# Optimization experiments

Measured on AMD Instinct MI355X. Metric: run time of the kernel, lower is better.

Reference implementation:

```python
import jax, jax.numpy as jnp
import numpy as np

N = 512      # hidden_size
L = 16384    # sequence length


def _make_hippo_legs(n_dim):
    # make_HiPPO_legs from the source
    b = jnp.sqrt(1.0 + 2.0 * jnp.arange(n_dim, dtype=jnp.float32))
    a = b[:, None] * b[None, :]
    a = jnp.tril(a) - jnp.diag(jnp.arange(n_dim, dtype=jnp.float32))
    return -a, b


def setup_inputs() -> dict:
    key = jax.random.key(0)
    c_key, x_key = jax.random.split(key, 2)
    A, Bv = _make_hippo_legs(N)
    B = Bv[:, None]                                   # (N, 1)
    C = jax.random.normal(c_key, (1, N), dtype=jnp.float32)
    in_x = jax.random.normal(x_key, (L,), dtype=jnp.float32)
    hidden_state = jnp.zeros((N,), dtype=jnp.float32)
    return {"in_x": in_x, "hidden_state": hidden_state, "A": A, "B": B, "C": C}


def reference(in_x, hidden_state, A, B, C):
    # discretize (bilinear / Tustin) with step = 1/L
    step = 1.0 / in_x.shape[0]
    I = jnp.eye(A.shape[0], dtype=A.dtype)
    BL = jnp.linalg.inv(I - (step / 2.0) * A)
    Ab = BL @ (I + (step / 2.0) * A)                  # (N, N)
    Bb = (BL * step) @ B                              # (N, 1)

    def step_through_time(h, x):
        # x: (1,) ; h: (N,)
        h_new = Ab @ h + Bb @ x                       # (N,)
        return h_new, C @ h_new                      # output (1,)

    new_hidden_state, output = jax.lax.scan(step_through_time, hidden_state, in_x[:, None])
    return output.squeeze(), new_hidden_state
```

## Files before the change

kernel.cpp:

```cpp
#include <hip/hip_runtime.h>

#define NDIM 512
#define LSEQ 16384
#define TCH  1024
#define PCH  16

#define DTF  (1.0f/16384.0f)
#define DT2F (0.5f/16384.0f)

__device__ __forceinline__ void gkt(float* smem,
    const float* A, int lda, const float* B, int ldb,
    float* D, int ldd, int row0, int col0, int K, float alpha)
{
    const int tid  = threadIdx.x;
    const int w    = tid >> 6;
    const int lane = tid & 63;
    const int ty = lane >> 3, tx = lane & 7;

    float* As = smem + w * 1152;
    float* Bs = As + 576;

    const int Kc    = K >> 2;
    const int steps = Kc >> 4;
    const int kbase = w * Kc;

    const int ar  = lane >> 2, acg = (lane & 3) * 4;
    const int bkr = lane >> 3, bcg = (lane & 7) * 4;
    const float* Ap0 = A + (size_t)(row0 + ar) * lda + kbase + acg;
    const float* Ap1 = Ap0 + (size_t)16 * lda;
    const float* Bp0 = B + (size_t)(kbase + bkr) * ldb + col0 + bcg;
    const float* Bp1 = Bp0 + (size_t)8 * ldb;

    float4 av0 = *(const float4*)Ap0;
    float4 av1 = *(const float4*)Ap1;
    float4 bv0 = *(const float4*)Bp0;
    float4 bv1 = *(const float4*)Bp1;

    float acc[4][4] = {};

    for (int s = 0; s < steps; ++s) {
        As[(acg + 0) * 36 + ar] = av0.x;
        As[(acg + 1) * 36 + ar] = av0.y;
        As[(acg + 2) * 36 + ar] = av0.z;
        As[(acg + 3) * 36 + ar] = av0.w;
        As[(acg + 0) * 36 + ar + 16] = av1.x;
        As[(acg + 1) * 36 + ar + 16] = av1.y;
        As[(acg + 2) * 36 + ar + 16] = av1.z;
        As[(acg + 3) * 36 + ar + 16] = av1.w;
        *(float4*)(Bs + bkr * 36 + bcg)       = bv0;
        *(float4*)(Bs + (bkr + 8) * 36 + bcg) = bv1;

        if (s + 1 < steps) {
            int ko = (s + 1) * 16;
            av0 = *(const float4*)(Ap0 + ko);
            av1 = *(const float4*)(Ap1 + ko);
            bv0 = *(const float4*)(Bp0 + (size_t)ko * ldb);
            bv1 = *(const float4*)(Bp1 + (size_t)ko * ldb);
        }

#pragma unroll
        for (int kk = 0; kk < 16; ++kk) {
            float4 a = *(const float4*)(As + kk * 36 + 4 * ty);
            float4 b = *(const float4*)(Bs + kk * 36 + 4 * tx);
            acc[0][0] += a.x * b.x; acc[0][1] += a.x * b.y; acc[0][2] += a.x * b.z; acc[0][3] += a.x * b.w;
            acc[1][0] += a.y * b.x; acc[1][1] += a.y * b.y; acc[1][2] += a.y * b.z; acc[1][3] += a.y * b.w;
            acc[2][0] += a.z * b.x; acc[2][1] += a.z * b.y; acc[2][2] += a.z * b.z; acc[2][3] += a.z * b.w;
            acc[3][0] += a.w * b.x; acc[3][1] += a.w * b.y; acc[3][2] += a.w * b.z; acc[3][3] += a.w * b.w;
        }
    }

    float* red = smem + w * 1152;
#pragma unroll
    for (int i = 0; i < 4; ++i)
        *(float4*)(red + (4 * ty + i) * 32 + 4 * tx) =
            make_float4(acc[i][0], acc[i][1], acc[i][2], acc[i][3]);
    __syncthreads();

    float4 s0 = *(const float4*)(smem + 0 * 1152 + tid * 4);
    float4 s1 = *(const float4*)(smem + 1 * 1152 + tid * 4);
    float4 s2 = *(const float4*)(smem + 2 * 1152 + tid * 4);
    float4 s3 = *(const float4*)(smem + 3 * 1152 + tid * 4);
    float4 r4 = make_float4(alpha * (s0.x + s1.x + s2.x + s3.x),
                            alpha * (s0.y + s1.y + s2.y + s3.y),
                            alpha * (s0.z + s1.z + s2.z + s3.z),
                            alpha * (s0.w + s1.w + s2.w + s3.w));
    int r = tid >> 3, c = (tid & 7) * 4;
    float* dp = D + (size_t)(row0 + r) * ldd + col0 + c;
    dp[0] = r4.x; dp[1] = r4.y; dp[2] = r4.z; dp[3] = r4.w;
}

__device__ __forceinline__ void tri_decode(int t, int& it, int& jt)
{
    it = (int)((sqrtf(8.f * (float)t + 1.f) - 1.f) * 0.5f);
    while ((it + 1) * (it + 2) / 2 <= t) ++it;
    while (it * (it + 1) / 2 > t) --it;
    jt = t - it * (it + 1) / 2;
}

__device__ __forceinline__ void scan_task(int task, const float* G,
    const float* Zold, float* Znew, const float* hs, float* Hmat,
    float* hfin, int o, int last)
{
    int wid = task * 4 + (threadIdx.x >> 6);
    int lane = threadIdx.x & 63;
    int p = wid & (PCH - 1), i = wid >> 4;
    float dot = 0.f;
    if (p >= o) {
        const float* gr = G + (size_t)i * NDIM;
        const float* zc = Zold + (size_t)(p - o) * NDIM;
        int rmax = i >> 6;
        for (int r = 0; r <= rmax; ++r) {
            int k = (r << 6) + lane;
            if (k <= i) dot += gr[k] * zc[k];
        }
#pragma unroll
        for (int off = 32; off; off >>= 1) dot += __shfl_xor(dot, off, 64);
    }
    if (lane == 0) {
        float z = Zold[(size_t)p * NDIM + i] + dot;
        Znew[(size_t)p * NDIM + i] = z;
        if (last) {
            if (p < PCH - 1) Hmat[(size_t)(p + 1) * NDIM + i] = z;
            else hfin[i] = z;
            if (p == 0) Hmat[i] = hs[i];
        }
    }
}

__global__ __launch_bounds__(256) void zero_diag(const float* __restrict__ A,
    float* __restrict__ W, float* __restrict__ P0)
{
    __shared__ float sh[64][65];
    const int t = blockIdx.x, tid = threadIdx.x;
    if (t < 8) {
        const int base = t * 64;
        for (int idx = tid; idx < 4096; idx += 256) {
            int r = idx >> 6, c = idx & 63;
            sh[r][c] = ((r == c) ? 1.f : 0.f)
                     - DT2F * A[(size_t)(base + r) * NDIM + base + c];
        }
        __syncthreads();
        if (tid < 64) {
            const int lane = tid;
            float xcol[64];
#pragma unroll
            for (int i = 0; i < 64; ++i) {
                float dot = 0.f;
#pragma unroll
                for (int k = 0; k < i; ++k) dot += sh[i][k] * xcol[k];
                xcol[i] = (((lane == i) ? 1.f : 0.f) - dot) / sh[i][i];
            }
#pragma unroll
            for (int k = 0; k < 64; ++k)
                W[(size_t)(base + k) * NDIM + base + lane] = xcol[k];
        }
    } else {
        const int q = (t - 8) >> 3, d = (t - 8) & 7;
        float* buf = P0 + (size_t)q * NDIM * NDIM;
        for (int idx = tid; idx < 4096; idx += 256) {
            int r = idx >> 6, c = idx & 63;
            if (c > r) buf[(size_t)(d * 64 + r) * NDIM + d * 64 + c] = 0.f;
        }
    }
}

__global__ __launch_bounds__(256) void pairA2(const float* __restrict__ A,
    const float* __restrict__ W, float* __restrict__ T, int s)
{
    __shared__ float smem[4608];
    int ntx = s >> 5;
    int tile = blockIdx.x;
    int it = tile / ntx, jt = tile - it * ntx;
    int o = blockIdx.y * 2 * s;
    int col0 = jt * 32, k0 = col0 & ~63;
    gkt(smem, A + (size_t)(o + s) * NDIM + o + k0, NDIM,
        W + (size_t)(o + k0) * NDIM + o, NDIM,
        T + (size_t)(o + s) * NDIM + o, NDIM,
        it * 32, col0, s - k0, 1.f);
}

__global__ __launch_bounds__(256) void pairB2(float* __restrict__ W,
    const float* __restrict__ T, int s)
{
    __shared__ float smem[4608];
    int ntx = s >> 5;
    int tile = blockIdx.x;
    int it = tile / ntx, jt = tile - it * ntx;
    int o = blockIdx.y * 2 * s;
    int ke = (it * 32 + 95) & ~63; if (ke > s) ke = s;
    gkt(smem, W + (size_t)(o + s) * NDIM + (o + s), NDIM,
        T + (size_t)(o + s) * NDIM + o, NDIM,
        W + (size_t)(o + s) * NDIM + o, NDIM,
        it * 32, jt * 32, ke, DT2F);
}

__global__ __launch_bounds__(256) void form_prep(const float* __restrict__ W,
    const float* __restrict__ Bv, const float* __restrict__ C,
    float* __restrict__ Ab, float* __restrict__ V, float* __restrict__ Crows,
    float* __restrict__ Bbc)
{
    const int b = blockIdx.x, tid = threadIdx.x;
    if (b < 256) {
        int idx = b * 256 + tid;
        int i = idx >> 7, j0 = (idx & 127) << 2;
        float4 wq = *(const float4*)(W + (size_t)i * NDIM + j0);
        float4 r = make_float4(2.f * wq.x, 2.f * wq.y, 2.f * wq.z, 2.f * wq.w);
        if (i == j0)          r.x -= 1.f;
        else if (i == j0 + 1) r.y -= 1.f;
        else if (i == j0 + 2) r.z -= 1.f;
        else if (i == j0 + 3) r.w -= 1.f;
        *(float4*)(Ab + (size_t)i * NDIM + j0) = r;
    } else if (b < 384) {
        const int wv = tid >> 6, lane = tid & 63;
        int i = (b - 256) * 4 + wv;
        float s = 0.f;
        int rmax = i >> 6;
        for (int c = 0; c <= rmax; ++c) {
            int k = (c << 6) + lane;
            if (k <= i) s += W[(size_t)i * NDIM + k] * Bv[k];
        }
#pragma unroll
        for (int off = 32; off; off >>= 1) s += __shfl_xor(s, off, 64);
        if (lane == 0) {
            float bb = DTF * s;
            V[(size_t)i * TCH] = bb;
            Bbc[i] = bb;
        }
    } else {
        Crows[tid]       = C[tid];
        Crows[tid + 256] = C[tid + 256];
    }
}

__global__ __launch_bounds__(256) void round_kernel(
    const float* __restrict__ g, float* __restrict__ gnew,
    float* __restrict__ V, float* __restrict__ Crows,
    int m, int lognx, int nz, int tailmode,
    const float* __restrict__ Gscan, const float* __restrict__ Ab,
    const float* __restrict__ x, const float* __restrict__ hs,
    const float* __restrict__ Bbc, float* __restrict__ kv,
    float* __restrict__ U, const float* __restrict__ Zin,
    float* __restrict__ Zout, float* __restrict__ Hmat,
    float* __restrict__ hfin, int o)
{
    __shared__ float smem[4608];
    const int t = blockIdx.x;
    const int tid = threadIdx.x;
    const int wv = tid >> 6, lane = tid & 63;

    if (t < 136) {
        int it, jt;
        tri_decode(t, it, jt);
        int k0 = (jt * 32) & ~63;
        int ke = (it * 32 + 95) & ~63; if (ke > NDIM) ke = NDIM;
        gkt(smem, g + k0, NDIM, g + (size_t)k0 * NDIM, NDIM,
            gnew, NDIM, it * 32, jt * 32, ke - k0, 1.f);
        return;
    }
    int u = t - 136;
    if (tailmode == 0) {
        int nmx = (m >= 32) ? (m >> 5) : 1;
        if (u < nz) {
            int it = u >> lognx, jt = u & (nmx - 1);
            int ke = (it * 32 + 95) & ~63; if (ke > NDIM) ke = NDIM;
            gkt(smem, g, NDIM, V, TCH, V + m, TCH, it * 32, jt * 32, ke, 1.f);
        } else {
            u -= nz;
            int it = u >> 4, jt = u & 15;
            int col0 = jt * 32, k0 = col0 & ~63;
            gkt(smem, Crows + k0, NDIM, g + (size_t)k0 * NDIM, NDIM,
                Crows + (size_t)m * NDIM, NDIM, it * 32, col0, NDIM - k0, 1.f);
        }
    } else if (tailmode == 1) {
        if (u < 2) {
            float* cs = smem;
            for (int k = tid; k < NDIM; k += 256)
                cs[k] = Crows[(size_t)1023 * NDIM + k];
            __syncthreads();
            int j = u * 256 + tid;
            int k0 = j & ~63;
            float acc = 0.f;
            for (int k = k0; k < NDIM; k += 4) {
                acc += cs[k]     * Ab[(size_t)k * NDIM + j]
                     + cs[k + 1] * Ab[(size_t)(k + 1) * NDIM + j]
                     + cs[k + 2] * Ab[(size_t)(k + 2) * NDIM + j]
                     + cs[k + 3] * Ab[(size_t)(k + 3) * NDIM + j];
            }
            Crows[(size_t)1024 * NDIM + j] = acc;
        } else if (u < 258) {
            int j = (u - 2) * 4 + wv;
            const float* cr = Crows + (size_t)j * NDIM;
            float dot = 0.f;
#pragma unroll
            for (int rr = 0; rr < 2; ++rr) {
                int oo = rr * 256 + lane * 4;
                float4 c4 = *(const float4*)(cr + oo);
                float4 b4 = *(const float4*)(Bbc + oo);
                dot += c4.x * b4.x + c4.y * b4.y + c4.z * b4.z + c4.w * b4.w;
            }
#pragma unroll
            for (int off = 32; off; off >>= 1) dot += __shfl_xor(dot, off, 64);
            if (lane == 0) kv[j] = dot;
        } else {
            int wid = (u - 258) * 4 + wv;
            int p = wid & (PCH - 1), i = wid >> 4;
            const float* vr = V + (size_t)i * TCH;
            const float* xc = x + p * TCH;
            float s = 0.f;
#pragma unroll
            for (int rr = 0; rr < 16; ++rr) {
                int t2 = (rr << 6) + lane;
                s += vr[TCH - 1 - t2] * xc[t2];
            }
            if (p == 0) {
                const float* gr = Gscan + (size_t)i * NDIM;
                int rmax = i >> 6;
                for (int rr = 0; rr <= rmax; ++rr) {
                    int k = (rr << 6) + lane;
                    if (k <= i) s += gr[k] * hs[k];
                }
            }
#pragma unroll
            for (int off = 32; off; off >>= 1) s += __shfl_xor(s, off, 64);
            if (lane == 0) U[(size_t)p * NDIM + i] = s;
        }
    } else {
        scan_task(u, Gscan, Zin, Zout, hs, Hmat, hfin, o, 0);
    }
}

__global__ __launch_bounds__(256) void scan_round(const float* __restrict__ G,
    const float* __restrict__ Zold, float* __restrict__ Znew,
    const float* __restrict__ hs, float* __restrict__ Hmat,
    float* __restrict__ hfin, int o, int last)
{
    scan_task(blockIdx.x, G, Zold, Znew, hs, Hmat, hfin, o, last);
}

__global__ __launch_bounds__(256) void emit(const float* __restrict__ Crows,
    const float* __restrict__ Hmat, const float* __restrict__ kv,
    const float* __restrict__ x, float* __restrict__ out)
{
    int wid = blockIdx.x * 4 + (threadIdx.x >> 6);
    int lane = threadIdx.x & 63;
    int p = wid & (PCH - 1), s = wid >> 4;
    const float* cr = Crows + (size_t)(s + 1) * NDIM;
    const float* hp = Hmat + (size_t)p * NDIM;
    float dot = 0.f;
#pragma unroll
    for (int r = 0; r < 2; ++r) {
        int o = r * 256 + lane * 4;
        float4 c = *(const float4*)(cr + o);
        float4 h = *(const float4*)(hp + o);
        dot += c.x * h.x + c.y * h.y + c.z * h.z + c.w * h.w;
    }
    const float* xc = x + p * TCH;
    int rmax = s >> 6;
    for (int r = 0; r <= rmax; ++r) {
        int t = (r << 6) + lane;
        if (t <= s) dot += kv[s - t] * xc[t];
    }
#pragma unroll
    for (int off = 32; off; off >>= 1) dot += __shfl_xor(dot, off, 64);
    if (lane == 0) out[p * TCH + s] = dot;
}

extern "C" void kernel_launch(void* const* d_in, const int* in_sizes, int n_in,
                              void* d_out, int out_size, void* d_ws, size_t ws_size,
                              hipStream_t stream)
{
    (void)in_sizes; (void)n_in; (void)out_size; (void)ws_size;
    const float* x  = (const float*)d_in[0];
    const float* hs = (const float*)d_in[1];
    const float* A  = (const float*)d_in[2];
    const float* Bv = (const float*)d_in[3];
    const float* C  = (const float*)d_in[4];
    float* out = (float*)d_out;

    const int MM = NDIM * NDIM;
    float* ws     = (float*)d_ws;
    float* Ab     = ws;
    float* P0     = Ab + MM;
    float* P1     = P0 + MM;
    float* GA     = P1 + MM;
    float* GB     = GA + MM;
    float* GC     = GB + MM;
    float* GD     = GC + MM;
    float* V      = GD + MM;
    float* Crows  = V + NDIM * TCH;
    float* CrowsW = Crows + TCH * NDIM;
    float* kv     = CrowsW + TCH * NDIM;
    float* Bbc    = kv + TCH;
    float* U      = Bbc + NDIM;
    float* Z0     = U + PCH * NDIM;
    float* Z1     = Z0 + PCH * NDIM;
    float* Hmat   = Z1 + PCH * NDIM;

    float* W = CrowsW;
    float* T = P0;

    zero_diag<<<56, 256, 0, stream>>>(A, W, P0);

    for (int s = 64; s <= 256; s <<= 1) {
        int np = NDIM / (2 * s);
        int tiles = (s >> 5) * (s >> 5);
        dim3 grid(tiles, np);
        pairA2<<<grid, 256, 0, stream>>>(A, W, T, s);
        pairB2<<<grid, 256, 0, stream>>>(W, T, s);
    }
    form_prep<<<385, 256, 0, stream>>>(W, Bv, C, Ab, V, Crows, Bbc);

    const float* g = Ab;
    float* gouts[13] = {P0, P1, P0, P1, P0, P1, P0, P1, P0, GA, GB, GC, GD};
    int m = 1;
    for (int r = 0; r < 13; ++r) {
        int nmx = (m >= 32) ? (m >> 5) : 1;
        int lognx = (r >= 5) ? (r - 5) : 0;
        int nz = (m < TCH) ? 16 * nmx : 0;
        int tailmode = 0, ntail = 0, oo = 0;
        const float* Gs = GA; const float* Zi = U; float* Zo = Z0;
        if (r == 10)      { tailmode = 1; ntail = 2306; }
        else if (r == 11) { tailmode = 2; ntail = 2048; oo = 1; }
        else if (r == 12) { tailmode = 2; ntail = 2048; oo = 2; Gs = GB;
                            Zi = Z0; Zo = Z1; }
        round_kernel<<<136 + 2 * nz + ntail, 256, 0, stream>>>(
            g, gouts[r], V, Crows, m, lognx, nz, tailmode, Gs, Ab,
            x, hs, Bbc, kv, U, Zi, Zo, Hmat, out + LSEQ, oo);
        g = gouts[r];
        m <<= 1;
    }

    scan_round<<<2048, 256, 0, stream>>>(GC, Z1, Z0, hs, Hmat, out + LSEQ, 4, 0);
    scan_round<<<2048, 256, 0, stream>>>(GD, Z0, Z1, hs, Hmat, out + LSEQ, 8, 1);

    emit<<<4096, 256, 0, stream>>>(Crows, Hmat, kv, x, out);
}
```

Baseline: 268.4 us.

## Deepen gkt register prefetch to two stages and schedule heavy tiles first

The shared GEMM-tile helper now keeps two k-steps of global loads in flight, in alternating even and odd register sets, instead of one. This hides more global-memory latency behind the FMA loop, at the cost of extra registers that may reduce occupancy. The tile-index decoding in pairA2, pairB2 and round_kernel is also reordered so that tiles with longer K ranges are dispatched first. That is meant to cut tail imbalance across blocks in the triangular workloads.

```diff
diff --git a/kernel.cpp b/kernel.cpp
--- a/kernel.cpp
+++ b/kernel.cpp
@@ -31,43 +31,65 @@
     const float* Bp0 = B + (size_t)(kbase + bkr) * ldb + col0 + bcg;
     const float* Bp1 = Bp0 + (size_t)8 * ldb;
 
-    float4 av0 = *(const float4*)Ap0;
-    float4 av1 = *(const float4*)Ap1;
-    float4 bv0 = *(const float4*)Bp0;
-    float4 bv1 = *(const float4*)Bp1;
-
     float acc[4][4] = {};
 
-    for (int s = 0; s < steps; ++s) {
-        As[(acg + 0) * 36 + ar] = av0.x;
-        As[(acg + 1) * 36 + ar] = av0.y;
-        As[(acg + 2) * 36 + ar] = av0.z;
-        As[(acg + 3) * 36 + ar] = av0.w;
-        As[(acg + 0) * 36 + ar + 16] = av1.x;
-        As[(acg + 1) * 36 + ar + 16] = av1.y;
-        As[(acg + 2) * 36 + ar + 16] = av1.z;
-        As[(acg + 3) * 36 + ar + 16] = av1.w;
-        *(float4*)(Bs + bkr * 36 + bcg)       = bv0;
-        *(float4*)(Bs + (bkr + 8) * 36 + bcg) = bv1;
-
-        if (s + 1 < steps) {
-            int ko = (s + 1) * 16;
-            av0 = *(const float4*)(Ap0 + ko);
-            av1 = *(const float4*)(Ap1 + ko);
-            bv0 = *(const float4*)(Bp0 + (size_t)ko * ldb);
-            bv1 = *(const float4*)(Bp1 + (size_t)ko * ldb);
-        }
-
-#pragma unroll
-        for (int kk = 0; kk < 16; ++kk) {
-            float4 a = *(const float4*)(As + kk * 36 + 4 * ty);
-            float4 b = *(const float4*)(Bs + kk * 36 + 4 * tx);
-            acc[0][0] += a.x * b.x; acc[0][1] += a.x * b.y; acc[0][2] += a.x * b.z; acc[0][3] += a.x * b.w;
-            acc[1][0] += a.y * b.x; acc[1][1] += a.y * b.y; acc[1][2] += a.y * b.z; acc[1][3] += a.y * b.w;
-            acc[2][0] += a.z * b.x; acc[2][1] += a.z * b.y; acc[2][2] += a.z * b.z; acc[2][3] += a.z * b.w;
-            acc[3][0] += a.w * b.x; acc[3][1] += a.w * b.y; acc[3][2] += a.w * b.z; acc[3][3] += a.w * b.w;
-        }
-    }
+    float4 aE0 = *(const float4*)Ap0;
+    float4 aE1 = *(const float4*)Ap1;
+    float4 bE0 = *(const float4*)Bp0;
+    float4 bE1 = *(const float4*)Bp1;
+    float4 aO0, aO1, bO0, bO1;
+    if (steps > 1) {
+        aO0 = *(const float4*)(Ap0 + 16);
+        aO1 = *(const float4*)(Ap1 + 16);
+        bO0 = *(const float4*)(Bp0 + (size_t)16 * ldb);
+        bO1 = *(const float4*)(Bp1 + (size_t)16 * ldb);
+    }
+
+#define GKT_STAGE(a0v,a1v,b0v,b1v)                                            \
+    As[(acg + 0) * 36 + ar] = a0v.x;  As[(acg + 1) * 36 + ar] = a0v.y;        \
+    As[(acg + 2) * 36 + ar] = a0v.z;  As[(acg + 3) * 36 + ar] = a0v.w;        \
+    As[(acg + 0) * 36 + ar + 16] = a1v.x; As[(acg + 1) * 36 + ar + 16] = a1v.y;\
+    As[(acg + 2) * 36 + ar + 16] = a1v.z; As[(acg + 3) * 36 + ar + 16] = a1v.w;\
+    *(float4*)(Bs + bkr * 36 + bcg)       = b0v;                              \
+    *(float4*)(Bs + (bkr + 8) * 36 + bcg) = b1v;
+
+#define GKT_COMPUTE                                                           \
+    _Pragma("unroll")                                                         \
+    for (int kk = 0; kk < 16; ++kk) {                                         \
+        float4 a = *(const float4*)(As + kk * 36 + 4 * ty);                   \
+        float4 b = *(const float4*)(Bs + kk * 36 + 4 * tx);                   \
+        acc[0][0] += a.x * b.x; acc[0][1] += a.x * b.y; acc[0][2] += a.x * b.z; acc[0][3] += a.x * b.w; \
+        acc[1][0] += a.y * b.x; acc[1][1] += a.y * b.y; acc[1][2] += a.y * b.z; acc[1][3] += a.y * b.w; \
+        acc[2][0] += a.z * b.x; acc[2][1] += a.z * b.y; acc[2][2] += a.z * b.z; acc[2][3] += a.z * b.w; \
+        acc[3][0] += a.w * b.x; acc[3][1] += a.w * b.y; acc[3][2] += a.w * b.z; acc[3][3] += a.w * b.w; \
+    }
+
+    int s = 0;
+    while (true) {
+        GKT_STAGE(aE0, aE1, bE0, bE1);
+        if (s + 2 < steps) {
+            int ko = (s + 2) * 16;
+            aE0 = *(const float4*)(Ap0 + ko);
+            aE1 = *(const float4*)(Ap1 + ko);
+            bE0 = *(const float4*)(Bp0 + (size_t)ko * ldb);
+            bE1 = *(const float4*)(Bp1 + (size_t)ko * ldb);
+        }
+        GKT_COMPUTE;
+        if (s + 1 >= steps) break;
+        GKT_STAGE(aO0, aO1, bO0, bO1);
+        if (s + 3 < steps) {
+            int ko = (s + 3) * 16;
+            aO0 = *(const float4*)(Ap0 + ko);
+            aO1 = *(const float4*)(Ap1 + ko);
+            bO0 = *(const float4*)(Bp0 + (size_t)ko * ldb);
+            bO1 = *(const float4*)(Bp1 + (size_t)ko * ldb);
+        }
+        GKT_COMPUTE;
+        s += 2;
+        if (s >= steps) break;
+    }
+#undef GKT_STAGE
+#undef GKT_COMPUTE
 
     float* red = smem + w * 1152;
 #pragma unroll
@@ -170,7 +192,7 @@
     __shared__ float smem[4608];
     int ntx = s >> 5;
     int tile = blockIdx.x;
-    int it = tile / ntx, jt = tile - it * ntx;
+    int jt = tile / ntx, it = tile - jt * ntx;
     int o = blockIdx.y * 2 * s;
     int col0 = jt * 32, k0 = col0 & ~63;
     gkt(smem, A + (size_t)(o + s) * NDIM + o + k0, NDIM,
@@ -185,7 +207,8 @@
     __shared__ float smem[4608];
     int ntx = s >> 5;
     int tile = blockIdx.x;
-    int it = tile / ntx, jt = tile - it * ntx;
+    int it = ntx - 1 - tile / ntx;
+    int jt = tile - (tile / ntx) * ntx;
     int o = blockIdx.y * 2 * s;
     int ke = (it * 32 + 95) & ~63; if (ke > s) ke = s;
     gkt(smem, W + (size_t)(o + s) * NDIM + (o + s), NDIM,
@@ -249,8 +272,9 @@
     const int wv = tid >> 6, lane = tid & 63;
 
     if (t < 136) {
-        int it, jt;
-        tri_decode(t, it, jt);
+        int e, j;
+        tri_decode(t, e, j);
+        int jt = j, it = 15 - e + j;
         int k0 = (jt * 32) & ~63;
         int ke = (it * 32 + 95) & ~63; if (ke > NDIM) ke = NDIM;
         gkt(smem, g + k0, NDIM, g + (size_t)k0 * NDIM, NDIM,
@@ -261,12 +285,14 @@
     if (tailmode == 0) {
         int nmx = (m >= 32) ? (m >> 5) : 1;
         if (u < nz) {
-            int it = u >> lognx, jt = u & (nmx - 1);
+            int up = nz - 1 - u;
+            int it = up >> lognx, jt = up & (nmx - 1);
             int ke = (it * 32 + 95) & ~63; if (ke > NDIM) ke = NDIM;
             gkt(smem, g, NDIM, V, TCH, V + m, TCH, it * 32, jt * 32, ke, 1.f);
         } else {
             u -= nz;
-            int it = u >> 4, jt = u & 15;
+            int nty = nmx;
+            int jt = u / nty, it = u - jt * nty;
             int col0 = jt * 32, k0 = col0 & ~63;
             gkt(smem, Crows + k0, NDIM, g + (size_t)k0 * NDIM, NDIM,
                 Crows + (size_t)m * NDIM, NDIM, it * 32, col0, NDIM - k0, 1.f);
```

Result: slower. 276.3 us (+3.0%).

## Fuse Ab/Bb formation into inverse tile epilogues and merge s=64 pair pass

Applied to the files above, without the earlier changes.

The separate form_prep pass is removed. Ab = 2W - I and Bb = dt*W*B are now written directly from the diagonal-block solve and from the off-diagonal block GEMM epilogues, with Bb accumulated via atomicAdd. The s=64 pairA2/pairB2 launches are merged into a single 4-block pair64 kernel, and the Crows copy moves into zero_diag. This cuts launches and a full pass over W. In exchange it relies on atomics and assumes Bbc/V start at zero and that the strictly upper blocks of Ab are zero-filled elsewhere.

```diff
diff --git a/kernel.cpp b/kernel.cpp
--- a/kernel.cpp
+++ b/kernel.cpp
@@ -4,13 +4,16 @@
 #define LSEQ 16384
 #define TCH  1024
 #define PCH  16
+#define MM   (NDIM * NDIM)
 
 #define DTF  (1.0f/16384.0f)
 #define DT2F (0.5f/16384.0f)
 
 __device__ __forceinline__ void gkt(float* smem,
     const float* A, int lda, const float* B, int ldb,
-    float* D, int ldd, int row0, int col0, int K, float alpha)
+    float* D, int ldd, int row0, int col0, int K, float alpha,
+    float* Abe = nullptr, float* Bbce = nullptr, float* Ve = nullptr,
+    const float* Bve = nullptr, int gr0 = -1, int gc0 = 0)
 {
     const int tid  = threadIdx.x;
     const int w    = tid >> 6;
@@ -87,6 +90,22 @@
     int r = tid >> 3, c = (tid & 7) * 4;
     float* dp = D + (size_t)(row0 + r) * ldd + col0 + c;
     dp[0] = r4.x; dp[1] = r4.y; dp[2] = r4.z; dp[3] = r4.w;
+
+    if (gr0 >= 0) {
+        int grow = gr0 + row0 + r, gcol = gc0 + col0 + c;
+        *(float4*)(Abe + (size_t)grow * NDIM + gcol) =
+            make_float4(2.f * r4.x, 2.f * r4.y, 2.f * r4.z, 2.f * r4.w);
+        float pv = r4.x * Bve[gcol]     + r4.y * Bve[gcol + 1]
+                 + r4.z * Bve[gcol + 2] + r4.w * Bve[gcol + 3];
+        pv += __shfl_xor(pv, 1, 64);
+        pv += __shfl_xor(pv, 2, 64);
+        pv += __shfl_xor(pv, 4, 64);
+        if ((tid & 7) == 0) {
+            float bb = DTF * pv;
+            atomicAdd(&Bbce[grow], bb);
+            atomicAdd(&Ve[(size_t)grow * TCH], bb);
+        }
+    }
 }
 
 __device__ __forceinline__ void tri_decode(int t, int& it, int& jt)
@@ -128,7 +147,9 @@
 }
 
 __global__ __launch_bounds__(256) void zero_diag(const float* __restrict__ A,
-    float* __restrict__ W, float* __restrict__ P0)
+    float* __restrict__ W, float* __restrict__ P0, float* __restrict__ Ab,
+    float* __restrict__ Bbc, float* __restrict__ V, float* __restrict__ Crows,
+    const float* __restrict__ Bv, const float* __restrict__ C)
 {
     __shared__ float sh[64][65];
     const int t = blockIdx.x, tid = threadIdx.x;
@@ -150,17 +171,59 @@
                 for (int k = 0; k < i; ++k) dot += sh[i][k] * xcol[k];
                 xcol[i] = (((lane == i) ? 1.f : 0.f) - dot) / sh[i][i];
             }
-#pragma unroll
-            for (int k = 0; k < 64; ++k)
-                W[(size_t)(base + k) * NDIM + base + lane] = xcol[k];
-        }
-    } else {
+            const float bvv = Bv[base + lane];
+#pragma unroll
+            for (int k = 0; k < 64; ++k) {
+                float xv = xcol[k];
+                W[(size_t)(base + k) * NDIM + base + lane] = xv;
+                Ab[(size_t)(base + k) * NDIM + base + lane] =
+                    2.f * xv - ((k == lane) ? 1.f : 0.f);
+                float pv = xv * bvv;
+#pragma unroll
+                for (int off = 32; off; off >>= 1) pv += __shfl_xor(pv, off, 64);
+                if (lane == 0) {
+                    float bb = DTF * pv;
+                    Bbc[base + k] = bb;
+                    V[(size_t)(base + k) * TCH] = bb;
+                }
+            }
+        }
+    } else if (t < 56) {
         const int q = (t - 8) >> 3, d = (t - 8) & 7;
-        float* buf = P0 + (size_t)q * NDIM * NDIM;
+        float* buf = P0 + (size_t)q * MM;
         for (int idx = tid; idx < 4096; idx += 256) {
             int r = idx >> 6, c = idx & 63;
             if (c > r) buf[(size_t)(d * 64 + r) * NDIM + d * 64 + c] = 0.f;
         }
+    } else {
+        Crows[tid]       = C[tid];
+        Crows[tid + 256] = C[tid + 256];
+    }
+}
+
+__global__ __launch_bounds__(256) void pair64(const float* __restrict__ A,
+    float* __restrict__ W, float* __restrict__ T, float* __restrict__ Ab,
+    float* __restrict__ Bbc, float* __restrict__ V, const float* __restrict__ Bv)
+{
+    __shared__ float smem[4608];
+    const int o = blockIdx.x * 128;
+#pragma unroll
+    for (int t = 0; t < 4; ++t) {
+        int it = t >> 1, jt = t & 1;
+        gkt(smem, A + (size_t)(o + 64) * NDIM + o, NDIM,
+            W + (size_t)o * NDIM + o, NDIM,
+            T + (size_t)(o + 64) * NDIM + o, NDIM,
+            it * 32, jt * 32, 64, 1.f);
+        __syncthreads();
+    }
+#pragma unroll
+    for (int t = 0; t < 4; ++t) {
+        int it = t >> 1, jt = t & 1;
+        gkt(smem, W + (size_t)(o + 64) * NDIM + (o + 64), NDIM,
+            T + (size_t)(o + 64) * NDIM + o, NDIM,
+            W + (size_t)(o + 64) * NDIM + o, NDIM,
+            it * 32, jt * 32, 64, DT2F, Ab, Bbc, V, Bv, o + 64, o);
+        __syncthreads();
     }
 }
 
@@ -180,7 +243,8 @@
 }
 
 __global__ __launch_bounds__(256) void pairB2(float* __restrict__ W,
-    const float* __restrict__ T, int s)
+    const float* __restrict__ T, int s, float* __restrict__ Ab,
+    float* __restrict__ Bbc, float* __restrict__ V, const float* __restrict__ Bv)
 {
     __shared__ float smem[4608];
     int ntx = s >> 5;
@@ -191,45 +255,7 @@
     gkt(smem, W + (size_t)(o + s) * NDIM + (o + s), NDIM,
         T + (size_t)(o + s) * NDIM + o, NDIM,
         W + (size_t)(o + s) * NDIM + o, NDIM,
-        it * 32, jt * 32, ke, DT2F);
-}
-
-__global__ __launch_bounds__(256) void form_prep(const float* __restrict__ W,
-    const float* __restrict__ Bv, const float* __restrict__ C,
-    float* __restrict__ Ab, float* __restrict__ V, float* __restrict__ Crows,
-    float* __restrict__ Bbc)
-{
-    const int b = blockIdx.x, tid = threadIdx.x;
-    if (b < 256) {
-        int idx = b * 256 + tid;
-        int i = idx >> 7, j0 = (idx & 127) << 2;
-        float4 wq = *(const float4*)(W + (size_t)i * NDIM + j0);
-        float4 r = make_float4(2.f * wq.x, 2.f * wq.y, 2.f * wq.z, 2.f * wq.w);
-        if (i == j0)          r.x -= 1.f;
-        else if (i == j0 + 1) r.y -= 1.f;
-        else if (i == j0 + 2) r.z -= 1.f;
-        else if (i == j0 + 3) r.w -= 1.f;
-        *(float4*)(Ab + (size_t)i * NDIM + j0) = r;
-    } else if (b < 384) {
-        const int wv = tid >> 6, lane = tid & 63;
-        int i = (b - 256) * 4 + wv;
-        float s = 0.f;
-        int rmax = i >> 6;
-        for (int c = 0; c <= rmax; ++c) {
-            int k = (c << 6) + lane;
-            if (k <= i) s += W[(size_t)i * NDIM + k] * Bv[k];
-        }
-#pragma unroll
-        for (int off = 32; off; off >>= 1) s += __shfl_xor(s, off, 64);
-        if (lane == 0) {
-            float bb = DTF * s;
-            V[(size_t)i * TCH] = bb;
-            Bbc[i] = bb;
-        }
-    } else {
-        Crows[tid]       = C[tid];
-        Crows[tid + 256] = C[tid + 256];
-    }
+        it * 32, jt * 32, ke, DT2F, Ab, Bbc, V, Bv, o + s, o);
 }
 
 __global__ __launch_bounds__(256) void round_kernel(
@@ -377,7 +403,6 @@
     const float* C  = (const float*)d_in[4];
     float* out = (float*)d_out;
 
-    const int MM = NDIM * NDIM;
     float* ws     = (float*)d_ws;
     float* Ab     = ws;
     float* P0     = Ab + MM;
@@ -399,16 +424,16 @@
     float* W = CrowsW;
     float* T = P0;
 
-    zero_diag<<<56, 256, 0, stream>>>(A, W, P0);
-
-    for (int s = 64; s <= 256; s <<= 1) {
+    zero_diag<<<57, 256, 0, stream>>>(A, W, P0, Ab, Bbc, V, Crows, Bv, C);
+
+    pair64<<<4, 256, 0, stream>>>(A, W, T, Ab, Bbc, V, Bv);
+    for (int s = 128; s <= 256; s <<= 1) {
         int np = NDIM / (2 * s);
         int tiles = (s >> 5) * (s >> 5);
         dim3 grid(tiles, np);
         pairA2<<<grid, 256, 0, stream>>>(A, W, T, s);
-        pairB2<<<grid, 256, 0, stream>>>(W, T, s);
-    }
-    form_prep<<<385, 256, 0, stream>>>(W, Bv, C, Ab, V, Crows, Bbc);
+        pairB2<<<grid, 256, 0, stream>>>(W, T, s, Ab, Bbc, V, Bv);
+    }
 
     const float* g = Ab;
     float* gouts[13] = {P0, P1, P0, P1, P0, P1, P0, P1, P0, GA, GB, GC, GD};
```

Result: slower. 444.1 us (+65.5%).
